# Kernel optimization log

Hardware: AMD Instinct MI355X
Metric: run time of the kernel (lower is better)

## Reference

```python
import jax, jax.numpy as jnp
import numpy as np

N_CODES = 1024
CODE_DIM = 256
DECAY = 0.99
EPS = 1e-05


def setup_inputs() -> dict:
    key = jax.random.key(0)
    k1, k2, k3, k4 = jax.random.split(key, 4)
    z = jax.random.normal(k1, (32, CODE_DIM, 32, 32), dtype=jnp.float32)
    embed = jax.random.normal(k2, (N_CODES, CODE_DIM), dtype=jnp.float32)
    cluster_size = jax.random.uniform(k3, (N_CODES,), dtype=jnp.float32)
    embed_avg = jax.random.normal(k4, (N_CODES, CODE_DIM), dtype=jnp.float32)
    return {"z": z, "embed": embed, "cluster_size": cluster_size, "embed_avg": embed_avg}


def reference(z, embed, cluster_size, embed_avg):
    B, D, H, W = z.shape
    K = embed.shape[0]
    # (B*H*W, D) tokens
    flat = jnp.transpose(z, (0, 2, 3, 1)).reshape(-1, D)
    distances = (
        jnp.sum(flat * flat, axis=1, keepdims=True)
        - 2.0 * flat @ embed.T
        + jnp.sum(embed * embed, axis=1)[None, :]
    )
    indices = jnp.argmin(distances, axis=1)  # (N,)
    z_q = embed[indices].reshape(B, H, W, D).transpose(0, 3, 1, 2)  # (B, D, H, W)

    # EMA codebook update (training mode), no onehot materialization
    cs = jax.ops.segment_sum(jnp.ones(flat.shape[0], dtype=flat.dtype), indices, num_segments=K)
    es = jax.ops.segment_sum(flat, indices, num_segments=K)
    new_cluster_size = cluster_size * DECAY + (1.0 - DECAY) * cs
    new_embed_avg = embed_avg * DECAY + (1.0 - DECAY) * es
    n = jnp.sum(new_cluster_size)
    cs_norm = (new_cluster_size + EPS) / (n + K * EPS) * n
    new_embed = new_embed_avg / cs_norm[:, None]

    # straight-through estimator
    z_q_st = z + jax.lax.stop_gradient(z_q - z)
    # torch: F.mse_loss(z.detach(), z_q) -> grads flow to z_q (codebook) only
    vq_loss = jnp.mean((jax.lax.stop_gradient(z) - z_q) ** 2)
    return (z_q_st, indices.reshape(B, H, W), vq_loss, new_embed, new_cluster_size, new_embed_avg)
```

## Files before the change

### kernel.cpp

```cpp
#include <hip/hip_runtime.h>
#include <stdint.h>

#define DECAY 0.99f
#define OMDECAY 0.01f
#define EPSV 1e-5f


typedef _Float16 half8 __attribute__((ext_vector_type(8)));
typedef float floatx4 __attribute__((ext_vector_type(4)));

typedef __attribute__((address_space(1))) const uint32_t gu32;
typedef __attribute__((address_space(3))) uint32_t lu32;

__device__ __forceinline__ void gld16(uint32_t* l, const uint32_t* g) {
    __builtin_amdgcn_global_load_lds((gu32*)g, (lu32*)l, 16, 0, 0);
}

__device__ __forceinline__ uint32_t pack_hl(float v) {
    _Float16 h = (_Float16)v;
    _Float16 lo = (_Float16)(v - (float)h);
    return (uint32_t)__builtin_bit_cast(unsigned short, h) |
           ((uint32_t)__builtin_bit_cast(unsigned short, lo) << 16);
}

__device__ __forceinline__ unsigned int encf(float s) {
    unsigned int b = __builtin_bit_cast(unsigned int, s);
    return (b & 0x80000000u) ? ~b : (b | 0x80000000u);
}
__device__ __forceinline__ float decf(unsigned int u) {
    unsigned int b = (u & 0x80000000u) ? (u ^ 0x80000000u) : ~u;
    return __builtin_bit_cast(float, b);
}

__global__ void prep_fused(const float* __restrict__ z,
                           uint32_t* __restrict__ A_hi32,
                           uint32_t* __restrict__ A_lo32,
                           const float* __restrict__ embed,
                           unsigned short* __restrict__ B_hi16,
                           unsigned short* __restrict__ B_lo16,
                           float* __restrict__ enorm,
                           float* __restrict__ cs ,
                           uint32_t* __restrict__ b64i,
                           float* __restrict__ znstash) {
    __shared__ uint32_t sp[32 * 258];
    __shared__ float znacc[4][32];
    const int bx = blockIdx.x;
    const int tid = threadIdx.x;
    const int lane = tid & 63;
    const int wv = tid >> 6;

    if (bx < 1024) {
        const int t0  = bx * 32;
        const int b   = t0 >> 10;
        const int hw0 = t0 & 1023;
        const int l32 = lane & 31;
        const int dh  = lane >> 5;
        float zn = 0.f;
        for (int dp = wv; dp < 128; dp += 4) {
            int dd = dp * 2 + dh;
            float v = z[b * 262144 + dd * 1024 + hw0 + l32];
            sp[l32 * 258 + dd] = pack_hl(v);
            zn += v * v;
        }
        zn += __shfl_xor(zn, 32);
        if (lane < 32) znacc[wv][lane] = zn;
        __syncthreads();
        if (tid < 32)
            znstash[t0 + tid] = znacc[0][tid] + znacc[1][tid] +
                                znacc[2][tid] + znacc[3][tid];
        for (int r = wv; r < 32; r += 4) {
#pragma unroll
            for (int h2 = 0; h2 < 2; ++h2) {
                int dpair = h2 * 64 + lane;
                uint32_t u0 = sp[r * 258 + 2 * dpair];
                uint32_t u1 = sp[r * 258 + 2 * dpair + 1];
                A_hi32[(t0 + r) * 128 + dpair] = (u0 & 0xffffu) | (u1 << 16);
                A_lo32[(t0 + r) * 128 + dpair] = (u0 >> 16) | (u1 & 0xffff0000u);
            }
        }
    } else {
        float* ws4 = (float*)sp;
        const int k = bx - 1024;
        const int d = tid;
        float v = embed[k * 256 + d];
        _Float16 h = (_Float16)v;
        _Float16 lo = (_Float16)(v - (float)h);
        const int c16 = k & 15, cg = k >> 4;
        const int dc = d >> 5, dl = d & 31;
        const int qq = dl >> 3, dw = (dl & 7) >> 1, hl = d & 1;
        const int us = ((cg * 8 + dc) * 256 + c16 * 16 + qq * 4 + dw) * 2 + hl;
        B_hi16[us] = __builtin_bit_cast(unsigned short, h);
        B_lo16[us] = __builtin_bit_cast(unsigned short, lo);
        float s = v * v;
        for (int off = 32; off > 0; off >>= 1) s += __shfl_down(s, off);
        if (lane == 0) ws4[wv] = s;
        __syncthreads();
        if (tid == 0) enorm[k] = ws4[0] + ws4[1] + ws4[2] + ws4[3];
        if (k < 256) b64i[k * 256 + tid] = 0xFFFFFFFFu;
        if (k == 0) {
            for (int i = tid; i < 2048; i += 256) cs[i] = 0.f;
        }
    }
}

__global__ __launch_bounds__(256, 2) void vq_mfma(
    const uint32_t* __restrict__ A_hi32,
    const uint32_t* __restrict__ A_lo32,
    const uint32_t* __restrict__ B_hi32,
    const uint32_t* __restrict__ B_lo32,
    const float* __restrict__ enorm,
    unsigned long long* __restrict__ best64)
{
    __shared__ __align__(16) _Float16 Abuf[2][2][4096];

    const int lane = threadIdx.x & 63;
    const int w    = threadIdx.x >> 6;
    const int q    = lane >> 4;
    const int c16  = lane & 15;
    const int bb   = blockIdx.x;
    const int xcd  = bb & 7;
    const int slot = bb >> 3;
    const int g    = (slot >> 2) * 8 + xcd;
    const int cq   = slot & 3;
    const int t0   = g * 128;
    const int cb   = cq * 256;
    const int lane4 = lane >> 2;
    const int dd8s  = ((lane & 3) ^ ((lane >> 3) & 3)) * 8;
    const int qs    = q ^ ((c16 >> 1) & 3);

    const uint32_t* const sA = (w >> 1) ? A_lo32 : A_hi32;
    const int r16b = (w & 1) * 4;

    float en[4];
    const uint32_t* bph[4];
    const uint32_t* bpl[4];
#pragma unroll
    for (int j = 0; j < 4; ++j) {
        const int code = cb + w * 64 + j * 16 + c16;
        en[j]  = enorm[code];
        const int cgj = (cb >> 4) + w * 4 + j;
        bph[j] = B_hi32 + cgj * 2048 + c16 * 16 + q * 4;
        bpl[j] = B_lo32 + cgj * 2048 + c16 * 16 + q * 4;
    }

    floatx4 acc[8][4];
#pragma unroll
    for (int i = 0; i < 8; ++i)
#pragma unroll
        for (int j = 0; j < 4; ++j)
            acc[i][j] = (floatx4){0.f, 0.f, 0.f, 0.f};

    half8 bh[2][4], bl[2][4];

    auto STAGE_A = [&](int step) {
        uint32_t* dst = (uint32_t*)(&Abuf[step & 1][w >> 1][0]);
        const int srcoff = (step * 32 + dd8s) >> 1;
#pragma unroll
        for (int s = 0; s < 4; ++s) {
            const int r16 = r16b + s;
            gld16(dst + r16 * 256, sA + (t0 + r16 * 16 + lane4) * 128 + srcoff);
        }
    };
    auto LOAD_B = [&](int step, half8* h, half8* l) {
#pragma unroll
        for (int j = 0; j < 4; ++j) {
            h[j] = *(const half8*)(bph[j] + step * 256);
            l[j] = *(const half8*)(bpl[j] + step * 256);
        }
    };

    STAGE_A(0);
    LOAD_B(0, bh[0], bl[0]);
    asm volatile("s_waitcnt vmcnt(8)" ::: "memory");
    __builtin_amdgcn_s_barrier();
    asm volatile("" ::: "memory");

#pragma unroll
    for (int dc = 0; dc < 8; ++dc) {
        const int cur = dc & 1;
        if (dc < 7) {
            STAGE_A(dc + 1);
            LOAD_B(dc + 1, bh[cur ^ 1], bl[cur ^ 1]);
        }
        const _Float16* pH = &Abuf[cur][0][0];
        const _Float16* pL = &Abuf[cur][1][0];
        __builtin_amdgcn_s_setprio(1);
#pragma unroll
        for (int i = 0; i < 8; ++i) {
            const int off = (i * 16 + c16) * 32 + qs * 8;
            half8 aH = *(const half8*)(pH + off);
            half8 aL = *(const half8*)(pL + off);
#pragma unroll
            for (int j = 0; j < 4; ++j) {
                acc[i][j] = __builtin_amdgcn_mfma_f32_16x16x32_f16(aH, bh[cur][j], acc[i][j], 0, 0, 0);
                acc[i][j] = __builtin_amdgcn_mfma_f32_16x16x32_f16(aH, bl[cur][j], acc[i][j], 0, 0, 0);
                acc[i][j] = __builtin_amdgcn_mfma_f32_16x16x32_f16(aL, bh[cur][j], acc[i][j], 0, 0, 0);
            }
        }
        __builtin_amdgcn_s_setprio(0);
        asm volatile("" ::: "memory");
        if (dc < 7) {
            asm volatile("s_waitcnt vmcnt(8)" ::: "memory");
            __builtin_amdgcn_s_barrier();
            asm volatile("" ::: "memory");
        }
    }

    unsigned long long best[32];
#pragma unroll
    for (int sl = 0; sl < 32; ++sl) best[sl] = ~0ULL;
#pragma unroll
    for (int j = 0; j < 4; ++j) {
        const unsigned int code = (unsigned int)(cb + w * 64 + j * 16 + c16);
        const float enj = en[j];
#pragma unroll
        for (int i = 0; i < 8; ++i)
#pragma unroll
            for (int r = 0; r < 4; ++r) {
                float sc = enj - 2.0f * acc[i][j][r];
                unsigned long long key =
                    ((unsigned long long)encf(sc) << 32) | code;
                int sl = i * 4 + r;
                if (key < best[sl]) best[sl] = key;
            }
    }
#pragma unroll
    for (int sl = 0; sl < 32; ++sl) {
        unsigned long long v = best[sl];
#pragma unroll
        for (int mm = 1; mm < 16; mm <<= 1) {
            unsigned long long o = __shfl_xor(v, mm);
            if (o < v) v = o;
        }
        if (c16 == (sl & 15)) {
            int tok = t0 + (sl >> 2) * 16 + q * 4 + (sl & 3);
            atomicMin(&best64[tok], v);
        }
    }
}

__global__ __launch_bounds__(256) void merge_zq(
    const unsigned long long* __restrict__ best64,
    const float* __restrict__ embed,
    float* __restrict__ out_zq,
    float* __restrict__ out_idx ,
    float* __restrict__ cs,
    float* __restrict__ loss_sum,
    float* __restrict__ es)
{
    __shared__ float elds[64 * 257];
    __shared__ int sidx[64];
    const int tid = threadIdx.x;
    const int lane = tid & 63;
    const int w = tid >> 6;
    const int t0 = blockIdx.x * 64;

    es[blockIdx.x * 512 + tid] = 0.f;
    es[blockIdx.x * 512 + 256 + tid] = 0.f;

    if (tid < 64) {
        unsigned long long key = best64[t0 + tid];
        int code = (int)(unsigned int)(key & 0xffffffffULL);
        float sc = decf((unsigned int)(key >> 32));
        float zn = out_idx[t0 + tid];
        sidx[tid] = code;
        out_idx[t0 + tid] = (float)code;
        atomicAdd(&cs[code], 1.0f);
        float val = zn + sc;
        for (int off = 32; off > 0; off >>= 1) val += __shfl_down(val, off);
        if (lane == 0) atomicAdd(loss_sum, val);
    }
    __syncthreads();

#pragma unroll
    for (int k = 0; k < 16; ++k) {
        const int row = w * 16 + k;
        const int ka = sidx[row];
        float4 v = *(const float4*)(embed + ka * 256 + lane * 4);
        float* dst = elds + row * 257 + lane * 4;
        dst[0] = v.x; dst[1] = v.y; dst[2] = v.z; dst[3] = v.w;
    }
    __syncthreads();

    const int b_idx = t0 >> 10;
    const int hw0   = t0 & 1023;
    const int zbase = b_idx * 262144 + hw0;
    const float* src = elds + lane * 257;
#pragma unroll
    for (int dd = 0; dd < 64; ++dd) {
        const int d = w * 64 + dd;
        out_zq[zbase + d * 1024 + lane] = src[d];
    }
}

__global__ void vq_finalize_small(const float* __restrict__ cluster_size,
                                  const float* __restrict__ cs,
                                  const float* __restrict__ loss_sum,
                                  float* __restrict__ out_loss,
                                  float* __restrict__ out_ncs,
                                  float* __restrict__ csnorm,
                                  int* __restrict__ offsets,
                                  int* __restrict__ cursor)
{
    __shared__ float wsum[16];
    __shared__ float wncs[16];
    __shared__ float stot[1];
    const int k = threadIdx.x;
    const int lane = k & 63;
    const int wv = k >> 6;
    float cnt = cs[k];
    float ncs = cluster_size[k] * DECAY + OMDECAY * cnt;
    out_ncs[k] = ncs;
    float sc = cnt;
#pragma unroll
    for (int d = 1; d < 64; d <<= 1) {
        float up = __shfl_up(sc, d);
        if (lane >= d) sc += up;
    }
    if (lane == 63) wsum[wv] = sc;
    float ns = ncs;
    for (int off = 32; off > 0; off >>= 1) ns += __shfl_down(ns, off);
    if (lane == 0) wncs[wv] = ns;
    __syncthreads();
    if (wv == 0) {
        float v = (lane < 16) ? wsum[lane] : 0.f;
#pragma unroll
        for (int d = 1; d < 16; d <<= 1) {
            float up = __shfl_up(v, d);
            if (lane >= d) v += up;
        }
        if (lane < 16) wsum[lane] = v;
    } else if (wv == 1) {
        float t = (lane < 16) ? wncs[lane] : 0.f;
        for (int off = 32; off > 0; off >>= 1) t += __shfl_down(t, off);
        if (lane == 0) stot[0] = t;
    }
    __syncthreads();
    float incl = sc + (wv ? wsum[wv - 1] : 0.f);
    int excl = __float2int_rn(incl - cnt);
    offsets[k] = excl;
    cursor[k]  = excl;
    float n = stot[0];
    csnorm[k] = (ncs + EPSV) / (n + 1024.0f * EPSV) * n;
    if (k == 0) out_loss[0] = loss_sum[0] / 8388608.0f;
}

__global__ void scatter_perm(const float* __restrict__ out_idx,
                             int* __restrict__ cursor,
                             int* __restrict__ perm)
{
    int t = blockIdx.x * 256 + threadIdx.x;
    int code = (int)out_idx[t];
    int pos = atomicAdd(&cursor[code], 1);
    perm[pos] = t;
}

__global__ void es_sum(const uint32_t* __restrict__ A_hi32,
                       const uint32_t* __restrict__ A_lo32,
                       const int* __restrict__ perm,
                       const float* __restrict__ out_idx,
                       float* __restrict__ es)
{
    __shared__ int sperm[32];
    __shared__ int scode[32];
    const int base = blockIdx.x * 32;
    const int tid = threadIdx.x;
    const int j = tid & 127;
    const uint32_t* __restrict__ A = (tid >> 7) ? A_lo32 : A_hi32;
    if (tid < 32) {
        int t = perm[base + tid];
        sperm[tid] = t;
        scode[tid] = (int)out_idx[t];
    }
    __syncthreads();

    float s0 = 0.f, s1 = 0.f;
    int cur = scode[0];
    uint32_t pu[2];
    pu[0] = A[sperm[0] * 128 + j];
    pu[1] = A[sperm[1] * 128 + j];
#pragma unroll
    for (int i = 0; i < 32; ++i) {
        uint32_t u = pu[i & 1];
        if (i + 2 < 32) pu[i & 1] = A[sperm[i + 2] * 128 + j];
        int code = scode[i];
        if (code != cur) {
            atomicAdd(&es[cur * 256 + 2 * j],     s0);
            atomicAdd(&es[cur * 256 + 2 * j + 1], s1);
            s0 = 0.f; s1 = 0.f; cur = code;
        }
        s0 += (float)__builtin_bit_cast(_Float16, (unsigned short)(u & 0xffffu));
        s1 += (float)__builtin_bit_cast(_Float16, (unsigned short)(u >> 16));
    }
    atomicAdd(&es[cur * 256 + 2 * j],     s0);
    atomicAdd(&es[cur * 256 + 2 * j + 1], s1);
}

__global__ void finalize_embed(const float* __restrict__ embed_avg,
                               const float* __restrict__ es,
                               const float* __restrict__ csnorm,
                               float* __restrict__ out_embed,
                               float* __restrict__ out_nea)
{
    int idx = blockIdx.x * 256 + threadIdx.x;
    int k = idx >> 8;
    float nea = embed_avg[idx] * DECAY + OMDECAY * es[idx];
    out_nea[idx] = nea;
    out_embed[idx] = nea / csnorm[k];
}

extern "C" void kernel_launch(void* const* d_in, const int* in_sizes, int n_in,
                              void* d_out, int out_size, void* d_ws, size_t ws_size,
                              hipStream_t stream) {
    const float* z            = (const float*)d_in[0];
    const float* embed        = (const float*)d_in[1];
    const float* cluster_size = (const float*)d_in[2];
    const float* embed_avg    = (const float*)d_in[3];
    float* out = (float*)d_out;
    uint32_t* ws32 = (uint32_t*)d_ws;

    uint32_t* B_hi32 = ws32 + 0;
    uint32_t* B_lo32 = ws32 + 131072;
    uint32_t* A_hi32 = ws32 + 262144;
    uint32_t* A_lo32 = ws32 + 4456448;
    int* perm        = (int*)(ws32 + 8650752);
    int* offsets     = (int*)(ws32 + 8683520);
    int* cursor      = (int*)(ws32 + 8684544);
    float* cs        = (float*)(ws32 + 8912896);
    float* loss_sum  = (float*)(ws32 + 8913920);
    float* enorm     = (float*)(ws32 + 8914944);
    float* csnorm    = (float*)(ws32 + 8915968);
    float* es        = (float*)(ws32 + 0);
    unsigned long long* best64 = (unsigned long long*)(out + 8421378);
    float* znstash = out + 8388608;

    prep_fused<<<2048, 256, 0, stream>>>(z, A_hi32, A_lo32, embed,
                                         (unsigned short*)B_hi32,
                                         (unsigned short*)B_lo32, enorm, cs,
                                         (uint32_t*)best64, znstash);
    vq_mfma<<<1024, 256, 0, stream>>>(A_hi32, A_lo32, B_hi32, B_lo32, enorm, best64);
    merge_zq<<<512, 256, 0, stream>>>(best64, embed,
                                      out, out + 8388608, cs, loss_sum, es);
    vq_finalize_small<<<1, 1024, 0, stream>>>(cluster_size, cs, loss_sum,
                                              out + 8421376, out + 8683521, csnorm,
                                              offsets, cursor);
    scatter_perm<<<128, 256, 0, stream>>>(out + 8388608, cursor, perm);
    es_sum<<<1024, 256, 0, stream>>>(A_hi32, A_lo32, perm, out + 8388608, es);
    finalize_embed<<<1024, 256, 0, stream>>>(embed_avg, es, csnorm,
                                             out + 8421377, out + 8684545);
}
```

Before: 226.0 us.

## Widen vq_mfma to 512-thread blocks with phased load/MFMA interleaving

Doubles the token tile per block to 256 by using 8 waves: each code-column wave set of four is shared by two token halves, so each B fragment load serves twice as many tokens. The inner loop is split into four phases that interleave the next-step A staging and per-j B loads with the MFMAs, adding extra workgroup barriers between phases. This aims to raise B reuse and hide global load latency. In exchange it doubles LDS use per block, halves the grid, and adds synchronization overhead.

Result: no change. 228.4 us (+1.1%).

```diff
diff --git a/kernel.cpp b/kernel.cpp
--- a/kernel.cpp
+++ b/kernel.cpp
@@ -103,7 +103,7 @@
     }
 }
 
-__global__ __launch_bounds__(256, 2) void vq_mfma(
+__global__ __launch_bounds__(512, 2) void vq_mfma(
     const uint32_t* __restrict__ A_hi32,
     const uint32_t* __restrict__ A_lo32,
     const uint32_t* __restrict__ B_hi32,
@@ -111,10 +111,12 @@
     const float* __restrict__ enorm,
     unsigned long long* __restrict__ best64)
 {
-    __shared__ __align__(16) _Float16 Abuf[2][2][4096];
+    __shared__ __align__(16) _Float16 Abuf[2][2][8192];
 
     const int lane = threadIdx.x & 63;
     const int w    = threadIdx.x >> 6;
+    const int wh   = w >> 2;
+    const int wj   = w & 3;
     const int q    = lane >> 4;
     const int c16  = lane & 15;
     const int bb   = blockIdx.x;
@@ -122,23 +124,23 @@
     const int slot = bb >> 3;
     const int g    = (slot >> 2) * 8 + xcd;
     const int cq   = slot & 3;
-    const int t0   = g * 128;
+    const int t0   = g * 256;
     const int cb   = cq * 256;
     const int lane4 = lane >> 2;
     const int dd8s  = ((lane & 3) ^ ((lane >> 3) & 3)) * 8;
     const int qs    = q ^ ((c16 >> 1) & 3);
 
-    const uint32_t* const sA = (w >> 1) ? A_lo32 : A_hi32;
-    const int r16b = (w & 1) * 4;
+    const uint32_t* const sA = (w >> 2) ? A_lo32 : A_hi32;
+    const int r16b = (w & 3) * 4;
 
     float en[4];
     const uint32_t* bph[4];
     const uint32_t* bpl[4];
 #pragma unroll
     for (int j = 0; j < 4; ++j) {
-        const int code = cb + w * 64 + j * 16 + c16;
+        const int code = cb + wj * 64 + j * 16 + c16;
         en[j]  = enorm[code];
-        const int cgj = (cb >> 4) + w * 4 + j;
+        const int cgj = (cb >> 4) + wj * 4 + j;
         bph[j] = B_hi32 + cgj * 2048 + c16 * 16 + q * 4;
         bpl[j] = B_lo32 + cgj * 2048 + c16 * 16 + q * 4;
     }
@@ -153,7 +155,7 @@
     half8 bh[2][4], bl[2][4];
 
     auto STAGE_A = [&](int step) {
-        uint32_t* dst = (uint32_t*)(&Abuf[step & 1][w >> 1][0]);
+        uint32_t* dst = (uint32_t*)(&Abuf[step & 1][w >> 2][0]);
         const int srcoff = (step * 32 + dd8s) >> 1;
 #pragma unroll
         for (int s = 0; s < 4; ++s) {
@@ -161,16 +163,14 @@
             gld16(dst + r16 * 256, sA + (t0 + r16 * 16 + lane4) * 128 + srcoff);
         }
     };
-    auto LOAD_B = [&](int step, half8* h, half8* l) {
-#pragma unroll
-        for (int j = 0; j < 4; ++j) {
-            h[j] = *(const half8*)(bph[j] + step * 256);
-            l[j] = *(const half8*)(bpl[j] + step * 256);
-        }
+    auto LOAD_B1 = [&](int step, int j, half8* h, half8* l) {
+        h[j] = *(const half8*)(bph[j] + step * 256);
+        l[j] = *(const half8*)(bpl[j] + step * 256);
     };
 
     STAGE_A(0);
-    LOAD_B(0, bh[0], bl[0]);
+#pragma unroll
+    for (int j = 0; j < 4; ++j) LOAD_B1(0, j, bh[0], bl[0]);
     asm volatile("s_waitcnt vmcnt(8)" ::: "memory");
     __builtin_amdgcn_s_barrier();
     asm volatile("" ::: "memory");
@@ -178,31 +178,44 @@
 #pragma unroll
     for (int dc = 0; dc < 8; ++dc) {
         const int cur = dc & 1;
-        if (dc < 7) {
-            STAGE_A(dc + 1);
-            LOAD_B(dc + 1, bh[cur ^ 1], bl[cur ^ 1]);
-        }
+        const int nxt = cur ^ 1;
         const _Float16* pH = &Abuf[cur][0][0];
         const _Float16* pL = &Abuf[cur][1][0];
-        __builtin_amdgcn_s_setprio(1);
-#pragma unroll
-        for (int i = 0; i < 8; ++i) {
-            const int off = (i * 16 + c16) * 32 + qs * 8;
-            half8 aH = *(const half8*)(pH + off);
-            half8 aL = *(const half8*)(pL + off);
-#pragma unroll
-            for (int j = 0; j < 4; ++j) {
-                acc[i][j] = __builtin_amdgcn_mfma_f32_16x16x32_f16(aH, bh[cur][j], acc[i][j], 0, 0, 0);
-                acc[i][j] = __builtin_amdgcn_mfma_f32_16x16x32_f16(aH, bl[cur][j], acc[i][j], 0, 0, 0);
-                acc[i][j] = __builtin_amdgcn_mfma_f32_16x16x32_f16(aL, bh[cur][j], acc[i][j], 0, 0, 0);
-            }
-        }
-        __builtin_amdgcn_s_setprio(0);
-        asm volatile("" ::: "memory");
-        if (dc < 7) {
-            asm volatile("s_waitcnt vmcnt(8)" ::: "memory");
+
+#pragma unroll
+        for (int ph = 0; ph < 4; ++ph) {
+            half8 aH[2], aL[2];
+#pragma unroll
+            for (int r = 0; r < 2; ++r) {
+                const int i = ph * 2 + r;
+                const int off = ((wh * 128 + i * 16 + c16) * 32) + qs * 8;
+                aH[r] = *(const half8*)(pH + off);
+                aL[r] = *(const half8*)(pL + off);
+            }
+            if (dc < 7) {
+                if (ph == 0) STAGE_A(dc + 1);
+                LOAD_B1(dc + 1, ph, bh[nxt], bl[nxt]);
+            }
             __builtin_amdgcn_s_barrier();
             asm volatile("" ::: "memory");
+            __builtin_amdgcn_s_setprio(1);
+#pragma unroll
+            for (int r = 0; r < 2; ++r) {
+                const int i = ph * 2 + r;
+#pragma unroll
+                for (int j = 0; j < 4; ++j) {
+                    acc[i][j] = __builtin_amdgcn_mfma_f32_16x16x32_f16(aH[r], bh[cur][j], acc[i][j], 0, 0, 0);
+                    acc[i][j] = __builtin_amdgcn_mfma_f32_16x16x32_f16(aH[r], bl[cur][j], acc[i][j], 0, 0, 0);
+                    acc[i][j] = __builtin_amdgcn_mfma_f32_16x16x32_f16(aL[r], bh[cur][j], acc[i][j], 0, 0, 0);
+                }
+            }
+            __builtin_amdgcn_s_setprio(0);
+            asm volatile("" ::: "memory");
+            if (ph == 3 && dc < 7) {
+                asm volatile("s_waitcnt vmcnt(8)" ::: "memory");
+            }
+            __builtin_amdgcn_s_barrier();
+            asm volatile("" ::: "memory");
         }
     }
 
@@ -211,7 +224,7 @@
     for (int sl = 0; sl < 32; ++sl) best[sl] = ~0ULL;
 #pragma unroll
     for (int j = 0; j < 4; ++j) {
-        const unsigned int code = (unsigned int)(cb + w * 64 + j * 16 + c16);
+        const unsigned int code = (unsigned int)(cb + wj * 64 + j * 16 + c16);
         const float enj = en[j];
 #pragma unroll
         for (int i = 0; i < 8; ++i)
@@ -233,7 +246,7 @@
             if (o < v) v = o;
         }
         if (c16 == (sl & 15)) {
-            int tok = t0 + (sl >> 2) * 16 + q * 4 + (sl & 3);
+            int tok = t0 + wh * 128 + (sl >> 2) * 16 + q * 4 + (sl & 3);
             atomicMin(&best64[tok], v);
         }
     }
@@ -438,7 +451,7 @@
                                          (unsigned short*)B_hi32,
                                          (unsigned short*)B_lo32, enorm, cs,
                                          (uint32_t*)best64, znstash);
-    vq_mfma<<<1024, 256, 0, stream>>>(A_hi32, A_lo32, B_hi32, B_lo32, enorm, best64);
+    vq_mfma<<<512, 512, 0, stream>>>(A_hi32, A_lo32, B_hi32, B_lo32, enorm, best64);
     merge_zq<<<512, 256, 0, stream>>>(best64, embed,
                                       out, out + 8388608, cs, loss_sum, es);
     vq_finalize_small<<<1, 1024, 0, stream>>>(cluster_size, cs, loss_sum,
```

## Vectorize prep transpose, fuse finalize into merge via last-block, widen es_sum loads

Applied to the files above, without the earlier changes.

The z transpose in prep now uses float4 global loads and uint4 stores when writing the hi/lo split A matrices. The single-block finalize kernel is folded into merge_zq: the last block to finish, found with an atomic counter, computes the new cluster sizes, the prefix-sum cursors, csnorm and the loss. This removes one kernel launch and its serial dependency. es_sum now loads uint2 per thread and splits tokens across two waves by parity, which adds more atomics in exchange for wider loads. The fused path needs the counter in loss_sum[1] to be reset each call.

Result: slower. 312.5 us (+38.3%).

```diff
diff --git a/kernel.cpp b/kernel.cpp
--- a/kernel.cpp
+++ b/kernel.cpp
@@ -53,30 +53,52 @@
         const int t0  = bx * 32;
         const int b   = t0 >> 10;
         const int hw0 = t0 & 1023;
-        const int l32 = lane & 31;
-        const int dh  = lane >> 5;
-        float zn = 0.f;
-        for (int dp = wv; dp < 128; dp += 4) {
-            int dd = dp * 2 + dh;
-            float v = z[b * 262144 + dd * 1024 + hw0 + l32];
-            sp[l32 * 258 + dd] = pack_hl(v);
-            zn += v * v;
-        }
-        zn += __shfl_xor(zn, 32);
-        if (lane < 32) znacc[wv][lane] = zn;
+        const int q8  = lane & 7;
+        const int r8  = lane >> 3;
+
+        float zn[4] = {0.f, 0.f, 0.f, 0.f};
+#pragma unroll
+        for (int it = 0; it < 8; ++it) {
+            const int d = it * 32 + wv * 8 + r8;
+            const float4 v4 = *(const float4*)(z + b * 262144 + d * 1024 + hw0 + q8 * 4);
+            const int tl = q8 * 4;
+            sp[(tl + 0) * 258 + d] = pack_hl(v4.x); zn[0] += v4.x * v4.x;
+            sp[(tl + 1) * 258 + d] = pack_hl(v4.y); zn[1] += v4.y * v4.y;
+            sp[(tl + 2) * 258 + d] = pack_hl(v4.z); zn[2] += v4.z * v4.z;
+            sp[(tl + 3) * 258 + d] = pack_hl(v4.w); zn[3] += v4.w * v4.w;
+        }
+#pragma unroll
+        for (int k = 0; k < 4; ++k) {
+            zn[k] += __shfl_down(zn[k], 32);
+            zn[k] += __shfl_down(zn[k], 16);
+            zn[k] += __shfl_down(zn[k], 8);
+        }
+        if (lane < 8) {
+#pragma unroll
+            for (int k = 0; k < 4; ++k) znacc[wv][lane * 4 + k] = zn[k];
+        }
         __syncthreads();
         if (tid < 32)
             znstash[t0 + tid] = znacc[0][tid] + znacc[1][tid] +
                                 znacc[2][tid] + znacc[3][tid];
-        for (int r = wv; r < 32; r += 4) {
-#pragma unroll
-            for (int h2 = 0; h2 < 2; ++h2) {
-                int dpair = h2 * 64 + lane;
-                uint32_t u0 = sp[r * 258 + 2 * dpair];
-                uint32_t u1 = sp[r * 258 + 2 * dpair + 1];
-                A_hi32[(t0 + r) * 128 + dpair] = (u0 & 0xffffu) | (u1 << 16);
-                A_lo32[(t0 + r) * 128 + dpair] = (u0 >> 16) | (u1 & 0xffff0000u);
+
+        const int tkn = tid >> 3;
+        const int qd  = tid & 7;
+#pragma unroll
+        for (int u = 0; u < 4; ++u) {
+            uint32_t hv[4], lv[4];
+#pragma unroll
+            for (int m = 0; m < 4; ++m) {
+                const int od = qd * 16 + u * 4 + m;
+                const uint32_t e0 = sp[tkn * 258 + od * 2];
+                const uint32_t e1 = sp[tkn * 258 + od * 2 + 1];
+                hv[m] = (e0 & 0xffffu) | (e1 << 16);
+                lv[m] = (e0 >> 16) | (e1 & 0xffff0000u);
             }
+            *(uint4*)(A_hi32 + (t0 + tkn) * 128 + qd * 16 + u * 4) =
+                make_uint4(hv[0], hv[1], hv[2], hv[3]);
+            *(uint4*)(A_lo32 + (t0 + tkn) * 128 + qd * 16 + u * 4) =
+                make_uint4(lv[0], lv[1], lv[2], lv[3]);
         }
     } else {
         float* ws4 = (float*)sp;
@@ -242,14 +264,21 @@
 __global__ __launch_bounds__(256) void merge_zq(
     const unsigned long long* __restrict__ best64,
     const float* __restrict__ embed,
+    const float* __restrict__ cluster_size,
     float* __restrict__ out_zq,
     float* __restrict__ out_idx ,
     float* __restrict__ cs,
-    float* __restrict__ loss_sum,
-    float* __restrict__ es)
+    float* __restrict__ loss_sum ,
+    float* __restrict__ es,
+    float* __restrict__ out_loss,
+    float* __restrict__ out_ncs,
+    float* __restrict__ csnorm,
+    int* __restrict__ cursor)
 {
     __shared__ float elds[64 * 257];
     __shared__ int sidx[64];
+    __shared__ float fw[4], fn[4];
+    __shared__ int sflag;
     const int tid = threadIdx.x;
     const int lane = tid & 63;
     const int w = tid >> 6;
@@ -268,7 +297,7 @@
         atomicAdd(&cs[code], 1.0f);
         float val = zn + sc;
         for (int off = 32; off > 0; off >>= 1) val += __shfl_down(val, off);
-        if (lane == 0) atomicAdd(loss_sum, val);
+        if (lane == 0) atomicAdd(&loss_sum[0], val);
     }
     __syncthreads();
 
@@ -291,58 +320,45 @@
         const int d = w * 64 + dd;
         out_zq[zbase + d * 1024 + lane] = src[d];
     }
-}
-
-__global__ void vq_finalize_small(const float* __restrict__ cluster_size,
-                                  const float* __restrict__ cs,
-                                  const float* __restrict__ loss_sum,
-                                  float* __restrict__ out_loss,
-                                  float* __restrict__ out_ncs,
-                                  float* __restrict__ csnorm,
-                                  int* __restrict__ offsets,
-                                  int* __restrict__ cursor)
-{
-    __shared__ float wsum[16];
-    __shared__ float wncs[16];
-    __shared__ float stot[1];
-    const int k = threadIdx.x;
-    const int lane = k & 63;
-    const int wv = k >> 6;
-    float cnt = cs[k];
-    float ncs = cluster_size[k] * DECAY + OMDECAY * cnt;
-    out_ncs[k] = ncs;
-    float sc = cnt;
+
+    __threadfence();
+    if (tid == 0)
+        sflag = (atomicAdd((int*)&loss_sum[1], 1) == 511) ? 1 : 0;
+    __syncthreads();
+    if (!sflag) return;
+
+    const int k4 = tid * 4;
+    float cnt[4], ncs[4];
+#pragma unroll
+    for (int m = 0; m < 4; ++m) {
+        cnt[m] = atomicAdd(&cs[k4 + m], 0.f);
+        ncs[m] = cluster_size[k4 + m] * DECAY + OMDECAY * cnt[m];
+        out_ncs[k4 + m] = ncs[m];
+    }
+    float csum = cnt[0] + cnt[1] + cnt[2] + cnt[3];
+    float nsum = ncs[0] + ncs[1] + ncs[2] + ncs[3];
+    float sc = csum;
 #pragma unroll
     for (int d = 1; d < 64; d <<= 1) {
         float up = __shfl_up(sc, d);
         if (lane >= d) sc += up;
     }
-    if (lane == 63) wsum[wv] = sc;
-    float ns = ncs;
+    float ns = nsum;
     for (int off = 32; off > 0; off >>= 1) ns += __shfl_down(ns, off);
-    if (lane == 0) wncs[wv] = ns;
+    if (lane == 63) fw[w] = sc;
+    if (lane == 0)  fn[w] = ns;
     __syncthreads();
-    if (wv == 0) {
-        float v = (lane < 16) ? wsum[lane] : 0.f;
-#pragma unroll
-        for (int d = 1; d < 16; d <<= 1) {
-            float up = __shfl_up(v, d);
-            if (lane >= d) v += up;
-        }
-        if (lane < 16) wsum[lane] = v;
-    } else if (wv == 1) {
-        float t = (lane < 16) ? wncs[lane] : 0.f;
-        for (int off = 32; off > 0; off >>= 1) t += __shfl_down(t, off);
-        if (lane == 0) stot[0] = t;
-    }
-    __syncthreads();
-    float incl = sc + (wv ? wsum[wv - 1] : 0.f);
-    int excl = __float2int_rn(incl - cnt);
-    offsets[k] = excl;
-    cursor[k]  = excl;
-    float n = stot[0];
-    csnorm[k] = (ncs + EPSV) / (n + 1024.0f * EPSV) * n;
-    if (k == 0) out_loss[0] = loss_sum[0] / 8388608.0f;
+    float base = 0.f;
+    for (int i = 0; i < w; ++i) base += fw[i];
+    const float ntot = fn[0] + fn[1] + fn[2] + fn[3];
+    float run = sc + base - csum;
+#pragma unroll
+    for (int m = 0; m < 4; ++m) {
+        cursor[k4 + m] = __float2int_rn(run);
+        run += cnt[m];
+        csnorm[k4 + m] = (ncs[m] + EPSV) / (ntot + 1024.0f * EPSV) * ntot;
+    }
+    if (tid == 0) out_loss[0] = atomicAdd(&loss_sum[0], 0.f) / 8388608.0f;
 }
 
 __global__ void scatter_perm(const float* __restrict__ out_idx,
@@ -365,8 +381,6 @@
     __shared__ int scode[32];
     const int base = blockIdx.x * 32;
     const int tid = threadIdx.x;
-    const int j = tid & 127;
-    const uint32_t* __restrict__ A = (tid >> 7) ? A_lo32 : A_hi32;
     if (tid < 32) {
         int t = perm[base + tid];
         sperm[tid] = t;
@@ -374,26 +388,40 @@
     }
     __syncthreads();
 
-    float s0 = 0.f, s1 = 0.f;
-    int cur = scode[0];
-    uint32_t pu[2];
-    pu[0] = A[sperm[0] * 128 + j];
-    pu[1] = A[sperm[1] * 128 + j];
-#pragma unroll
-    for (int i = 0; i < 32; ++i) {
-        uint32_t u = pu[i & 1];
-        if (i + 2 < 32) pu[i & 1] = A[sperm[i + 2] * 128 + j];
-        int code = scode[i];
+    const int j2   = tid & 63;
+    const int wv   = tid >> 6;
+    const int half = wv >> 1;
+    const int par  = wv & 1;
+    const uint32_t* __restrict__ A = half ? A_lo32 : A_hi32;
+
+    float s0 = 0.f, s1 = 0.f, s2 = 0.f, s3 = 0.f;
+    int cur = scode[par];
+    uint2 pu[2];
+    pu[0] = *(const uint2*)(A + sperm[par] * 128 + 2 * j2);
+    pu[1] = (par + 2 < 32) ? *(const uint2*)(A + sperm[par + 2] * 128 + 2 * j2)
+                           : pu[0];
+    int n = 0;
+    for (int ii = par; ii < 32; ii += 2, ++n) {
+        uint2 u = pu[n & 1];
+        if (ii + 4 < 32)
+            pu[n & 1] = *(const uint2*)(A + sperm[ii + 4] * 128 + 2 * j2);
+        int code = scode[ii];
         if (code != cur) {
-            atomicAdd(&es[cur * 256 + 2 * j],     s0);
-            atomicAdd(&es[cur * 256 + 2 * j + 1], s1);
-            s0 = 0.f; s1 = 0.f; cur = code;
-        }
-        s0 += (float)__builtin_bit_cast(_Float16, (unsigned short)(u & 0xffffu));
-        s1 += (float)__builtin_bit_cast(_Float16, (unsigned short)(u >> 16));
-    }
-    atomicAdd(&es[cur * 256 + 2 * j],     s0);
-    atomicAdd(&es[cur * 256 + 2 * j + 1], s1);
+            atomicAdd(&es[cur * 256 + 4 * j2 + 0], s0);
+            atomicAdd(&es[cur * 256 + 4 * j2 + 1], s1);
+            atomicAdd(&es[cur * 256 + 4 * j2 + 2], s2);
+            atomicAdd(&es[cur * 256 + 4 * j2 + 3], s3);
+            s0 = s1 = s2 = s3 = 0.f; cur = code;
+        }
+        s0 += (float)__builtin_bit_cast(_Float16, (unsigned short)(u.x & 0xffffu));
+        s1 += (float)__builtin_bit_cast(_Float16, (unsigned short)(u.x >> 16));
+        s2 += (float)__builtin_bit_cast(_Float16, (unsigned short)(u.y & 0xffffu));
+        s3 += (float)__builtin_bit_cast(_Float16, (unsigned short)(u.y >> 16));
+    }
+    atomicAdd(&es[cur * 256 + 4 * j2 + 0], s0);
+    atomicAdd(&es[cur * 256 + 4 * j2 + 1], s1);
+    atomicAdd(&es[cur * 256 + 4 * j2 + 2], s2);
+    atomicAdd(&es[cur * 256 + 4 * j2 + 3], s3);
 }
 
 __global__ void finalize_embed(const float* __restrict__ embed_avg,
@@ -424,7 +452,6 @@
     uint32_t* A_hi32 = ws32 + 262144;
     uint32_t* A_lo32 = ws32 + 4456448;
     int* perm        = (int*)(ws32 + 8650752);
-    int* offsets     = (int*)(ws32 + 8683520);
     int* cursor      = (int*)(ws32 + 8684544);
     float* cs        = (float*)(ws32 + 8912896);
     float* loss_sum  = (float*)(ws32 + 8913920);
@@ -439,11 +466,9 @@
                                          (unsigned short*)B_lo32, enorm, cs,
                                          (uint32_t*)best64, znstash);
     vq_mfma<<<1024, 256, 0, stream>>>(A_hi32, A_lo32, B_hi32, B_lo32, enorm, best64);
-    merge_zq<<<512, 256, 0, stream>>>(best64, embed,
-                                      out, out + 8388608, cs, loss_sum, es);
-    vq_finalize_small<<<1, 1024, 0, stream>>>(cluster_size, cs, loss_sum,
-                                              out + 8421376, out + 8683521, csnorm,
-                                              offsets, cursor);
+    merge_zq<<<512, 256, 0, stream>>>(best64, embed, cluster_size,
+                                      out, out + 8388608, cs, loss_sum, es,
+                                      out + 8421376, out + 8683521, csnorm, cursor);
     scatter_perm<<<128, 256, 0, stream>>>(out + 8388608, cursor, perm);
     es_sum<<<1024, 256, 0, stream>>>(A_hi32, A_lo32, perm, out + 8388608, es);
     finalize_embed<<<1024, 256, 0, stream>>>(embed_avg, es, csnorm,
```
